# Performance work log

Measured on AMD Instinct MI355X. Metric: run time of the kernel, lower is better.

The kernel has to match this reference:

```python
import jax, jax.numpy as jnp
import numpy as np

N_NODES = 50000
NUM_FEATURES = 64
HIDDEN = 512
NUM_CLASSES = 2
N_EDGES = 800000
BN_EPS = 1e-5


def setup_inputs() -> dict:
    key = jax.random.key(0)
    ks = jax.random.split(key, 10)
    x = jax.random.normal(ks[0], (N_NODES, NUM_FEATURES), dtype=jnp.float32)
    edge_index = jax.random.randint(ks[1], (2, N_EDGES), 0, N_NODES, dtype=jnp.int64)
    # GINConv MLP: Linear(F,H) -> ReLU -> Linear(H,H)
    W1 = jax.random.normal(ks[2], (NUM_FEATURES, HIDDEN), dtype=jnp.float32) * 0.05
    b1 = jnp.zeros((HIDDEN,), dtype=jnp.float32)
    W2 = jax.random.normal(ks[3], (HIDDEN, HIDDEN), dtype=jnp.float32) * 0.05
    b2 = jnp.zeros((HIDDEN,), dtype=jnp.float32)
    # BatchNorm1d(HIDDEN) affine params
    gamma = jnp.ones((HIDDEN,), dtype=jnp.float32)
    beta = jnp.zeros((HIDDEN,), dtype=jnp.float32)
    # classifier: Linear(HIDDEN, NUM_CLASSES)
    Wc = jax.random.normal(ks[4], (HIDDEN, NUM_CLASSES), dtype=jnp.float32) * 0.05
    bc = jnp.zeros((NUM_CLASSES,), dtype=jnp.float32)
    return {"x": x, "edge_index": edge_index, "W1": W1, "b1": b1,
            "W2": W2, "b2": b2, "gamma": gamma, "beta": beta,
            "Wc": Wc, "bc": bc}


def reference(x, edge_index, W1, b1, W2, b2, gamma, beta, Wc, bc):
    # NOTE: the original torch forward returns inside the loop, so exactly ONE
    # GINConv layer runs, followed by batchnorm, relu, dropout(p=0), classifier.
    src, dst = edge_index[0], edge_index[1]
    # GINConv (eps=0): h_i = MLP(x_i + sum_{j -> i} x_j)
    agg = jax.ops.segment_sum(x[src], dst, num_segments=x.shape[0])  # [N, F]
    h = x + agg
    h = jax.nn.relu(h @ W1 + b1) @ W2 + b2  # [N, H]
    # BatchNorm1d in training mode: normalize with batch statistics (biased var)
    mean = jnp.mean(h, axis=0)
    var = jnp.var(h, axis=0)
    h = (h - mean) * jax.lax.rsqrt(var + BN_EPS) * gamma + beta
    h = jax.nn.relu(h)
    # dropout p=0.0 is a no-op
    return h @ Wc + bc  # [N, NUM_CLASSES]
```

## Files before the change

kernel.cpp:

```cpp
#include <hip/hip_runtime.h>
#include <hip/hip_bf16.h>

#define NN 50000
#define MP 50176
#define NF 64
#define NH 512
#define NE 800000
#define NBK 196
#define EBCAP 8192
#define ABLK 391
#define MB 392
#define GRID (MB * 4)
#define CPX (GRID / 8)

typedef __attribute__((ext_vector_type(8))) short bf16x8;
typedef __attribute__((ext_vector_type(4))) float f32x4;

#define GLOAD16(g, l)                                                        \
    __builtin_amdgcn_global_load_lds(                                        \
        (const __attribute__((address_space(1))) unsigned int*)(g),          \
        (__attribute__((address_space(3))) unsigned int*)(l), 16, 0, 0)

__global__ void detect_idx(const int* __restrict__ ei, int* __restrict__ flag) {
    if (threadIdx.x == 0 && blockIdx.x == 0) {
        int any = 0;
        for (int i = 0; i < 32; ++i) any |= ei[2 * i + 1];
        *flag = (any == 0) ? 1 : 0;
    }
}

__global__ __launch_bounds__(256) void bucketA(const void* __restrict__ eiv,
                                               const int* __restrict__ flag,
                                               int* __restrict__ bcnt,
                                               int* __restrict__ ebS,
                                               int* __restrict__ ebD) {
    __shared__ int hist[NBK];
    __shared__ int lcur[NBK];
    const int tid = threadIdx.x;
    const int chunk = blockIdx.x * 2048;
    const int lim = min(2048, NE - chunk);
    const bool is64 = (*flag != 0);
    const long long* ei64 = (const long long*)eiv;
    const int* ei32 = (const int*)eiv;

    for (int i = tid; i < NBK; i += 256) hist[i] = 0;
    __syncthreads();
    for (int i = tid; i < lim; i += 256) {
        int d = is64 ? (int)ei64[NE + chunk + i] : ei32[NE + chunk + i];
        atomicAdd(&hist[d >> 8], 1);
    }
    __syncthreads();
    for (int i = tid; i < NBK; i += 256) {
        int c = hist[i];
        lcur[i] = c ? atomicAdd(&bcnt[i], c) : 0;
    }
    __syncthreads();
    for (int i = tid; i < lim; i += 256) {
        int s, d;
        if (is64) { s = (int)ei64[chunk + i]; d = (int)ei64[NE + chunk + i]; }
        else      { s = ei32[chunk + i];      d = ei32[NE + chunk + i]; }
        int b = d >> 8;
        int p = atomicAdd(&lcur[b], 1);
        ebS[b * EBCAP + p] = s;
        ebD[b * EBCAP + p] = d;
    }
}

__global__ __launch_bounds__(256) void scan_bsum(const int* __restrict__ bsum,
                                                 int* __restrict__ boff) {
    __shared__ int sm[256];
    int tid = threadIdx.x;
    int v = (tid < NBK) ? bsum[tid] : 0;
    sm[tid] = v;
    __syncthreads();
    int acc = v;
#pragma unroll
    for (int off = 1; off < 256; off <<= 1) {
        int t = (tid >= off) ? sm[tid - off] : 0;
        __syncthreads();
        acc += t;
        sm[tid] = acc;
        __syncthreads();
    }
    if (tid < NBK) boff[tid] = acc - v;
}

__global__ __launch_bounds__(256) void bucketB(const int* __restrict__ ebS,
                                               const int* __restrict__ ebD,
                                               const int* __restrict__ bcnt,
                                               const int* __restrict__ bbase,
                                               int* __restrict__ rowptr,
                                               int* __restrict__ csr) {
    __shared__ int hist[256], sm[256], curs[256];
    const int b = blockIdx.x;
    const int tid = threadIdx.x;
    const int n0 = b << 8;
    const int cnt = bcnt[b];
    const int base = bbase[b];

    hist[tid] = 0;
    __syncthreads();
    for (int i = tid; i < cnt; i += 256)
        atomicAdd(&hist[ebD[b * EBCAP + i] & 255], 1);
    __syncthreads();
    int v = hist[tid];
    sm[tid] = v;
    __syncthreads();
    int acc = v;
#pragma unroll
    for (int off = 1; off < 256; off <<= 1) {
        int t = (tid >= off) ? sm[tid - off] : 0;
        __syncthreads();
        acc += t;
        sm[tid] = acc;
        __syncthreads();
    }
    int excl = acc - v;
    if (n0 + tid < NN) rowptr[n0 + tid] = base + excl;
    curs[tid] = excl;
    __syncthreads();
    for (int i = tid; i < cnt; i += 256) {
        int s = ebS[b * EBCAP + i];
        int d = ebD[b * EBCAP + i] & 255;
        int lp = atomicAdd(&curs[d], 1);
        csr[base + lp] = s;
    }
    if (b == 0 && tid == 0) rowptr[NN] = NE;
}

__global__ __launch_bounds__(256) void cvt_x(const float* __restrict__ x,
                                             __hip_bfloat16* __restrict__ xb) {
    int t = blockIdx.x * 256 + threadIdx.x;
    if (t >= NN * NF / 4) return;
    float4 v = *(const float4*)&x[t * 4];
    union { ushort4 u; __hip_bfloat16 h[4]; } o;
    o.h[0] = __float2bfloat16(v.x);
    o.h[1] = __float2bfloat16(v.y);
    o.h[2] = __float2bfloat16(v.z);
    o.h[3] = __float2bfloat16(v.w);
    *(ushort4*)&xb[t * 4] = o.u;
}

__global__ __launch_bounds__(256) void gather(const __hip_bfloat16* __restrict__ xb,
                                              const int* __restrict__ rowptr,
                                              const int* __restrict__ csr,
                                              __hip_bfloat16* __restrict__ h0b) {
    int n = blockIdx.x * 4 + (threadIdx.x >> 6);
    int lane = threadIdx.x & 63;
    if (n >= MP) return;
    if (n >= NN) {
        h0b[(long long)n * NF + lane] = __float2bfloat16(0.f);
        return;
    }
    float acc = __bfloat162float(xb[(long long)n * NF + lane]);
    int e = rowptr[n], e1 = rowptr[n + 1];
    for (; e + 4 <= e1; e += 4) {
        int s0 = csr[e], s1 = csr[e + 1], s2 = csr[e + 2], s3 = csr[e + 3];
        float v0 = __bfloat162float(xb[(long long)s0 * NF + lane]);
        float v1 = __bfloat162float(xb[(long long)s1 * NF + lane]);
        float v2 = __bfloat162float(xb[(long long)s2 * NF + lane]);
        float v3 = __bfloat162float(xb[(long long)s3 * NF + lane]);
        acc += (v0 + v1) + (v2 + v3);
    }
    for (; e < e1; ++e) acc += __bfloat162float(xb[(long long)csr[e] * NF + lane]);
    h0b[(long long)n * NF + lane] = __float2bfloat16(acc);
}

__global__ __launch_bounds__(256) void cvt_wt(const float* __restrict__ W,
                                              __hip_bfloat16* __restrict__ WT,
                                              int K, int N) {
    int t = blockIdx.x * 256 + threadIdx.x;
    if (t >= K * N) return;
    int n = t % N, k = t / N;
    WT[n * K + k] = __float2bfloat16(W[t]);
}

__global__ __launch_bounds__(256) void gemm1_direct(const __hip_bfloat16* __restrict__ A,
                                                    const __hip_bfloat16* __restrict__ BT,
                                                    const float* __restrict__ bias,
                                                    __hip_bfloat16* __restrict__ C) {
    const int orig = blockIdx.x;
    const int L = (orig & 7) * CPX + (orig >> 3);
    const int mb = L >> 2, nb = L & 3;

    const int tid = threadIdx.x;
    const int lane = tid & 63;
    const int w = tid >> 6;
    const int wm = w >> 1, wn = w & 1;
    const long long rbase = (long long)mb * 128;
    const int nbase = nb * 128;
    const int lo = lane & 15, hi = lane >> 4;

    f32x4 acc[4][4];
#pragma unroll
    for (int i = 0; i < 4; ++i)
#pragma unroll
        for (int j = 0; j < 4; ++j) acc[i][j] = (f32x4){0.f, 0.f, 0.f, 0.f};

#pragma unroll
    for (int ks = 0; ks < 2; ++ks) {
        bf16x8 af[4], bfr[4];
#pragma unroll
        for (int mi = 0; mi < 4; ++mi)
            af[mi] = *(const bf16x8*)&A[(rbase + wm * 64 + mi * 16 + lo) * NF +
                                        ks * 32 + hi * 8];
#pragma unroll
        for (int ni = 0; ni < 4; ++ni)
            bfr[ni] = *(const bf16x8*)&BT[(long long)(nbase + wn * 64 + ni * 16 + lo) * NF +
                                          ks * 32 + hi * 8];
#pragma unroll
        for (int mi = 0; mi < 4; ++mi)
#pragma unroll
            for (int ni = 0; ni < 4; ++ni)
                acc[mi][ni] = __builtin_amdgcn_mfma_f32_16x16x32_bf16(
                    af[mi], bfr[ni], acc[mi][ni], 0, 0, 0);
    }

    const int col0 = nbase + wn * 64 + lo;
    const long long row00 = rbase + wm * 64 + hi * 4;
#pragma unroll
    for (int ni = 0; ni < 4; ++ni) {
        int col = col0 + ni * 16;
        float bv = bias[col];
#pragma unroll
        for (int mi = 0; mi < 4; ++mi) {
            long long r0 = row00 + mi * 16;
#pragma unroll
            for (int r = 0; r < 4; ++r) {
                float v = fmaxf(acc[mi][ni][r] + bv, 0.f);
                C[(r0 + r) * NH + col] = __float2bfloat16(v);
            }
        }
    }
}

__global__ __launch_bounds__(256) void gemm2_db(const __hip_bfloat16* __restrict__ A,
                                                const __hip_bfloat16* __restrict__ BT,
                                                const float* __restrict__ bias,
                                                __hip_bfloat16* __restrict__ C,
                                                float* __restrict__ partial) {
    constexpr int BK = 64;
    __shared__ __align__(16) char smem[65536];
    float* smsum = (float*)smem;
    float* smsq  = (float*)(smem + 2048);

    const int orig = blockIdx.x;
    const int L = (orig & 7) * CPX + (orig >> 3);
    const int mb = L >> 2, nb = L & 3;

    const int tid = threadIdx.x;
    const int lane = tid & 63;
    const int w = tid >> 6;
    const int wm = w >> 1, wn = w & 1;
    const long long rbase = (long long)mb * 128;
    const int nbase = nb * 128;
    const int r8  = lane >> 3;
    const int swc = (lane & 7) ^ r8;
    const int key = lane & 7;
    const int lo = lane & 15, hi = lane >> 4;

    const __hip_bfloat16* gaBase =
        A + (rbase + w * 32 + r8) * (long long)NH + swc * 8;
    const __hip_bfloat16* gbBase =
        BT + (long long)(nbase + w * 32 + r8) * NH + swc * 8;
    const int laOff = (w * 32) * BK;

    auto STAGE = [&](int s, int kb) {
        __hip_bfloat16* la = (__hip_bfloat16*)(smem + s * 32768) + laOff;
        __hip_bfloat16* lb = (__hip_bfloat16*)(smem + s * 32768 + 16384) + laOff;
#pragma unroll
        for (int t = 0; t < 4; ++t)
            GLOAD16(gaBase + kb + (long long)t * 8 * NH, la + t * 8 * BK);
#pragma unroll
        for (int t = 0; t < 4; ++t)
            GLOAD16(gbBase + kb + (long long)t * 8 * NH, lb + t * 8 * BK);
    };

    f32x4 acc[4][4];
#pragma unroll
    for (int i = 0; i < 4; ++i)
#pragma unroll
        for (int j = 0; j < 4; ++j) acc[i][j] = (f32x4){0.f, 0.f, 0.f, 0.f};

    STAGE(0, 0);
    STAGE(1, BK);

#pragma unroll
    for (int t = 0; t < 8; ++t) {
        if (t == 7) { asm volatile("s_waitcnt vmcnt(0)" ::: "memory"); }
        else        { asm volatile("s_waitcnt vmcnt(8)" ::: "memory"); }
        __builtin_amdgcn_s_barrier();
        __builtin_amdgcn_sched_barrier(0);

        const __hip_bfloat16* Ac = (const __hip_bfloat16*)(smem + (t & 1) * 32768);
        const __hip_bfloat16* Bc = Ac + 8192;
#pragma unroll
        for (int ks = 0; ks < 2; ++ks) {
            bf16x8 af[4], bfr[4];
#pragma unroll
            for (int mi = 0; mi < 4; ++mi)
                af[mi] = *(const bf16x8*)&Ac[(wm * 64 + mi * 16 + lo) * BK +
                                             (((ks * 4 + hi) ^ key) * 8)];
#pragma unroll
            for (int ni = 0; ni < 4; ++ni)
                bfr[ni] = *(const bf16x8*)&Bc[(wn * 64 + ni * 16 + lo) * BK +
                                              (((ks * 4 + hi) ^ key) * 8)];
#pragma unroll
            for (int mi = 0; mi < 4; ++mi)
#pragma unroll
                for (int ni = 0; ni < 4; ++ni)
                    acc[mi][ni] = __builtin_amdgcn_mfma_f32_16x16x32_bf16(
                        af[mi], bfr[ni], acc[mi][ni], 0, 0, 0);
        }
        __builtin_amdgcn_sched_barrier(0);
        __builtin_amdgcn_s_barrier();
        __builtin_amdgcn_sched_barrier(0);
        if (t < 6) STAGE(t & 1, (t + 2) * BK);
    }

    __syncthreads();
    if (tid < 128) { smsum[tid] = 0.f; smsq[tid] = 0.f; }
    __syncthreads();
    const int col0 = nbase + wn * 64 + lo;
    const long long row00 = rbase + wm * 64 + hi * 4;
#pragma unroll
    for (int ni = 0; ni < 4; ++ni) {
        int col = col0 + ni * 16;
        float bv = bias[col];
        float s = 0.f, q = 0.f;
#pragma unroll
        for (int mi = 0; mi < 4; ++mi) {
            long long r0 = row00 + mi * 16;
#pragma unroll
            for (int r = 0; r < 4; ++r) {
                float v = acc[mi][ni][r] + bv;
                C[(r0 + r) * NH + col] = __float2bfloat16(v);
                if ((r0 + r) < NN) { s += v; q += v * v; }
            }
        }
        s += __shfl_xor(s, 16); s += __shfl_xor(s, 32);
        q += __shfl_xor(q, 16); q += __shfl_xor(q, 32);
        if (lane < 16) {
            atomicAdd(&smsum[wn * 64 + ni * 16 + lane], s);
            atomicAdd(&smsq[wn * 64 + ni * 16 + lane], q);
        }
    }
    __syncthreads();
    if (tid < 128) {
        partial[mb * 1024 + nbase + tid] = smsum[tid];
        partial[mb * 1024 + 512 + nbase + tid] = smsq[tid];
    }
}

__global__ __launch_bounds__(256) void stats_reduce(const float* __restrict__ partial,
                                                    float* __restrict__ stats) {
    int j = blockIdx.x * 256 + threadIdx.x;
    float s = 0.f;
    for (int mb = 0; mb < MB; ++mb) s += partial[mb * 1024 + j];
    stats[j] = s;
}

__global__ __launch_bounds__(256) void bn_cls(const __hip_bfloat16* __restrict__ h2b,
                                              const float* __restrict__ stats,
                                              const float* __restrict__ gamma,
                                              const float* __restrict__ beta,
                                              const float* __restrict__ Wc,
                                              const float* __restrict__ bc,
                                              float* __restrict__ out) {
    int tid = threadIdx.x;
    int lane = tid & 63;
    int k0 = lane * 8;
    float sc[8], sh[8], w0[8], w1[8];
#pragma unroll
    for (int j = 0; j < 8; ++j) {
        int k = k0 + j;
        float mean = stats[k] * (1.0f / NN);
        float var = stats[512 + k] * (1.0f / NN) - mean * mean;
        float rs = rsqrtf(var + 1e-5f);
        float s = gamma[k] * rs;
        sc[j] = s;
        sh[j] = beta[k] - mean * s;
        w0[j] = Wc[2 * k];
        w1[j] = Wc[2 * k + 1];
    }
    float bc0 = bc[0], bc1 = bc[1];
    int wid = blockIdx.x * 4 + (tid >> 6);
    int nw = gridDim.x * 4;
    for (int row = wid; row < NN; row += nw) {
        bf16x8 v8 = *(const bf16x8*)&h2b[(long long)row * NH + k0];
        float a0 = 0.f, a1 = 0.f;
#pragma unroll
        for (int j = 0; j < 8; ++j) {
            float v = __bfloat162float(((const __hip_bfloat16*)&v8)[j]);
            float hn = fmaxf(fmaf(v, sc[j], sh[j]), 0.f);
            a0 = fmaf(hn, w0[j], a0);
            a1 = fmaf(hn, w1[j], a1);
        }
#pragma unroll
        for (int off = 32; off; off >>= 1) {
            a0 += __shfl_xor(a0, off);
            a1 += __shfl_xor(a1, off);
        }
        if (lane == 0) {
            out[(long long)row * 2 + 0] = a0 + bc0;
            out[(long long)row * 2 + 1] = a1 + bc1;
        }
    }
}

extern "C" void kernel_launch(void* const* d_in, const int* in_sizes, int n_in,
                              void* d_out, int out_size, void* d_ws, size_t ws_size,
                              hipStream_t stream) {
    const float* x     = (const float*)d_in[0];
    const void*  ei    = d_in[1];
    const float* W1    = (const float*)d_in[2];
    const float* b1    = (const float*)d_in[3];
    const float* W2    = (const float*)d_in[4];
    const float* b2    = (const float*)d_in[5];
    const float* gamma = (const float*)d_in[6];
    const float* beta  = (const float*)d_in[7];
    const float* Wc    = (const float*)d_in[8];
    const float* bc    = (const float*)d_in[9];
    float* out = (float*)d_out;

    char* base = (char*)d_ws;
    size_t o = 0;
    auto alloc = [&](size_t bytes) {
        char* p = base + o;
        o = (o + bytes + 255) & ~(size_t)255;
        return p;
    };
    __hip_bfloat16* h0b     = (__hip_bfloat16*)alloc((size_t)MP * NF * 2);
    __hip_bfloat16* h1b     = (__hip_bfloat16*)alloc((size_t)MP * NH * 2);
    __hip_bfloat16* h2b     = (__hip_bfloat16*)alloc((size_t)MP * NH * 2);
    __hip_bfloat16* xb      = (__hip_bfloat16*)alloc((size_t)NN * NF * 2);
    __hip_bfloat16* w1t     = (__hip_bfloat16*)alloc((size_t)NH * NF * 2);
    __hip_bfloat16* w2t     = (__hip_bfloat16*)alloc((size_t)NH * NH * 2);
    int*            ebS     = (int*)alloc((size_t)NBK * EBCAP * 4);
    int*            ebD     = (int*)alloc((size_t)NBK * EBCAP * 4);
    int*            bcnt    = (int*)alloc(256 * 4);
    int*            bbase   = (int*)alloc(256 * 4);
    int*            rowptr  = (int*)alloc((size_t)(NN + 1) * 4);
    int*            csr     = (int*)alloc((size_t)NE * 4);
    float*          partial = (float*)alloc((size_t)MB * 1024 * 4);
    float*          stats   = (float*)alloc(1024 * 4);
    int*            flag    = (int*)alloc(256);

    hipMemsetAsync(bcnt, 0, NBK * 4, stream);
    detect_idx<<<1, 1, 0, stream>>>((const int*)ei, flag);

    bucketA<<<ABLK, 256, 0, stream>>>(ei, flag, bcnt, ebS, ebD);
    scan_bsum<<<1, 256, 0, stream>>>(bcnt, bbase);
    bucketB<<<NBK, 256, 0, stream>>>(ebS, ebD, bcnt, bbase, rowptr, csr);

    cvt_x<<<(NN * NF / 4 + 255) / 256, 256, 0, stream>>>(x, xb);
    gather<<<MP / 4, 256, 0, stream>>>(xb, rowptr, csr, h0b);

    cvt_wt<<<(NF * NH + 255) / 256, 256, 0, stream>>>(W1, w1t, NF, NH);
    cvt_wt<<<(NH * NH + 255) / 256, 256, 0, stream>>>(W2, w2t, NH, NH);

    gemm1_direct<<<GRID, 256, 0, stream>>>(h0b, w1t, b1, h1b);
    gemm2_db<<<GRID, 256, 0, stream>>>(h1b, w2t, b2, h2b, partial);

    stats_reduce<<<4, 256, 0, stream>>>(partial, stats);
    bn_cls<<<512, 256, 0, stream>>>(h2b, stats, gamma, beta, Wc, bc, out);
}
```

Before: 179.8 us.

## Pack edge bucket entries, merge conversion kernels, stage GEMM1 A tile in LDS

Bucketed edges are stored as one packed int (local dst in the high bits, src in the low 16 bits) instead of two separate arrays, which halves bucket traffic. The x, W1 and W2 bf16 conversions are merged into one launch to save launch overhead. GEMM1 now loads its A tile into swizzled LDS with async global-to-LDS copies and preloads the B fragments into registers. Packing src into 16 bits is only correct for node indices below 65536, so it relies on N_NODES=50000.

```diff
diff --git a/kernel.cpp b/kernel.cpp
--- a/kernel.cpp
+++ b/kernel.cpp
@@ -32,8 +32,7 @@
 __global__ __launch_bounds__(256) void bucketA(const void* __restrict__ eiv,
                                                const int* __restrict__ flag,
                                                int* __restrict__ bcnt,
-                                               int* __restrict__ ebS,
-                                               int* __restrict__ ebD) {
+                                               int* __restrict__ ebP) {
     __shared__ int hist[NBK];
     __shared__ int lcur[NBK];
     const int tid = threadIdx.x;
@@ -61,8 +60,7 @@
         else      { s = ei32[chunk + i];      d = ei32[NE + chunk + i]; }
         int b = d >> 8;
         int p = atomicAdd(&lcur[b], 1);
-        ebS[b * EBCAP + p] = s;
-        ebD[b * EBCAP + p] = d;
+        ebP[b * EBCAP + p] = ((d & 255) << 16) | s;
     }
 }
 
@@ -85,8 +83,7 @@
     if (tid < NBK) boff[tid] = acc - v;
 }
 
-__global__ __launch_bounds__(256) void bucketB(const int* __restrict__ ebS,
-                                               const int* __restrict__ ebD,
+__global__ __launch_bounds__(256) void bucketB(const int* __restrict__ ebP,
                                                const int* __restrict__ bcnt,
                                                const int* __restrict__ bbase,
                                                int* __restrict__ rowptr,
@@ -101,7 +98,7 @@
     hist[tid] = 0;
     __syncthreads();
     for (int i = tid; i < cnt; i += 256)
-        atomicAdd(&hist[ebD[b * EBCAP + i] & 255], 1);
+        atomicAdd(&hist[(ebP[b * EBCAP + i] >> 16) & 255], 1);
     __syncthreads();
     int v = hist[tid];
     sm[tid] = v;
@@ -120,25 +117,41 @@
     curs[tid] = excl;
     __syncthreads();
     for (int i = tid; i < cnt; i += 256) {
-        int s = ebS[b * EBCAP + i];
-        int d = ebD[b * EBCAP + i] & 255;
-        int lp = atomicAdd(&curs[d], 1);
-        csr[base + lp] = s;
+        int p = ebP[b * EBCAP + i];
+        int lp = atomicAdd(&curs[(p >> 16) & 255], 1);
+        csr[base + lp] = p & 0xFFFF;
     }
     if (b == 0 && tid == 0) rowptr[NN] = NE;
 }
 
-__global__ __launch_bounds__(256) void cvt_x(const float* __restrict__ x,
-                                             __hip_bfloat16* __restrict__ xb) {
-    int t = blockIdx.x * 256 + threadIdx.x;
-    if (t >= NN * NF / 4) return;
-    float4 v = *(const float4*)&x[t * 4];
-    union { ushort4 u; __hip_bfloat16 h[4]; } o;
-    o.h[0] = __float2bfloat16(v.x);
-    o.h[1] = __float2bfloat16(v.y);
-    o.h[2] = __float2bfloat16(v.z);
-    o.h[3] = __float2bfloat16(v.w);
-    *(ushort4*)&xb[t * 4] = o.u;
+#define XBLK  (NN * NF / 4 / 256)
+#define W1BLK (NF * NH / 256)
+#define W2BLK (NH * NH / 256)
+__global__ __launch_bounds__(256) void cvt_all(const float* __restrict__ x,
+                                               const float* __restrict__ W1,
+                                               const float* __restrict__ W2,
+                                               __hip_bfloat16* __restrict__ xb,
+                                               __hip_bfloat16* __restrict__ w1t,
+                                               __hip_bfloat16* __restrict__ w2t) {
+    int bb = blockIdx.x;
+    if (bb < XBLK) {
+        int t = bb * 256 + threadIdx.x;
+        float4 v = *(const float4*)&x[t * 4];
+        union { ushort4 u; __hip_bfloat16 h[4]; } o;
+        o.h[0] = __float2bfloat16(v.x);
+        o.h[1] = __float2bfloat16(v.y);
+        o.h[2] = __float2bfloat16(v.z);
+        o.h[3] = __float2bfloat16(v.w);
+        *(ushort4*)&xb[t * 4] = o.u;
+    } else if (bb < XBLK + W1BLK) {
+        int t = (bb - XBLK) * 256 + threadIdx.x;
+        int n = t % NH, k = t / NH;
+        w1t[n * NF + k] = __float2bfloat16(W1[t]);
+    } else {
+        int t = (bb - XBLK - W1BLK) * 256 + threadIdx.x;
+        int n = t % NH, k = t / NH;
+        w2t[n * NH + k] = __float2bfloat16(W2[t]);
+    }
 }
 
 __global__ __launch_bounds__(256) void gather(const __hip_bfloat16* __restrict__ xb,
@@ -166,19 +179,11 @@
     h0b[(long long)n * NF + lane] = __float2bfloat16(acc);
 }
 
-__global__ __launch_bounds__(256) void cvt_wt(const float* __restrict__ W,
-                                              __hip_bfloat16* __restrict__ WT,
-                                              int K, int N) {
-    int t = blockIdx.x * 256 + threadIdx.x;
-    if (t >= K * N) return;
-    int n = t % N, k = t / N;
-    WT[n * K + k] = __float2bfloat16(W[t]);
-}
-
-__global__ __launch_bounds__(256) void gemm1_direct(const __hip_bfloat16* __restrict__ A,
+__global__ __launch_bounds__(256) void gemm1_staged(const __hip_bfloat16* __restrict__ A,
                                                     const __hip_bfloat16* __restrict__ BT,
                                                     const float* __restrict__ bias,
                                                     __hip_bfloat16* __restrict__ C) {
+    __shared__ __hip_bfloat16 As[128 * 64];
     const int orig = blockIdx.x;
     const int L = (orig & 7) * CPX + (orig >> 3);
     const int mb = L >> 2, nb = L & 3;
@@ -189,8 +194,27 @@
     const int wm = w >> 1, wn = w & 1;
     const long long rbase = (long long)mb * 128;
     const int nbase = nb * 128;
+    const int r8  = lane >> 3;
+    const int swc = (lane & 7) ^ r8;
+    const int key = lane & 7;
     const int lo = lane & 15, hi = lane >> 4;
 
+    {
+        const __hip_bfloat16* ga = A + (rbase + w * 32 + r8) * NF + swc * 8;
+        __hip_bfloat16* la = As + (w * 32) * 64;
+#pragma unroll
+        for (int t = 0; t < 4; ++t)
+            GLOAD16(ga + t * 8 * NF, la + t * 8 * 64);
+    }
+    bf16x8 bfr[2][4];
+#pragma unroll
+    for (int ks = 0; ks < 2; ++ks)
+#pragma unroll
+        for (int ni = 0; ni < 4; ++ni)
+            bfr[ks][ni] = *(const bf16x8*)&BT[(nbase + wn * 64 + ni * 16 + lo) * NF +
+                                             ks * 32 + hi * 8];
+    __syncthreads();
+
     f32x4 acc[4][4];
 #pragma unroll
     for (int i = 0; i < 4; ++i)
@@ -199,21 +223,17 @@
 
 #pragma unroll
     for (int ks = 0; ks < 2; ++ks) {
-        bf16x8 af[4], bfr[4];
+        bf16x8 af[4];
 #pragma unroll
         for (int mi = 0; mi < 4; ++mi)
-            af[mi] = *(const bf16x8*)&A[(rbase + wm * 64 + mi * 16 + lo) * NF +
-                                        ks * 32 + hi * 8];
-#pragma unroll
-        for (int ni = 0; ni < 4; ++ni)
-            bfr[ni] = *(const bf16x8*)&BT[(long long)(nbase + wn * 64 + ni * 16 + lo) * NF +
-                                          ks * 32 + hi * 8];
+            af[mi] = *(const bf16x8*)&As[(wm * 64 + mi * 16 + lo) * 64 +
+                                         (((ks * 4 + hi) ^ key) * 8)];
 #pragma unroll
         for (int mi = 0; mi < 4; ++mi)
 #pragma unroll
             for (int ni = 0; ni < 4; ++ni)
                 acc[mi][ni] = __builtin_amdgcn_mfma_f32_16x16x32_bf16(
-                    af[mi], bfr[ni], acc[mi][ni], 0, 0, 0);
+                    af[mi], bfr[ks][ni], acc[mi][ni], 0, 0, 0);
     }
 
     const int col0 = nbase + wn * 64 + lo;
@@ -436,8 +456,7 @@
     __hip_bfloat16* xb      = (__hip_bfloat16*)alloc((size_t)NN * NF * 2);
     __hip_bfloat16* w1t     = (__hip_bfloat16*)alloc((size_t)NH * NF * 2);
     __hip_bfloat16* w2t     = (__hip_bfloat16*)alloc((size_t)NH * NH * 2);
-    int*            ebS     = (int*)alloc((size_t)NBK * EBCAP * 4);
-    int*            ebD     = (int*)alloc((size_t)NBK * EBCAP * 4);
+    int*            ebP     = (int*)alloc((size_t)NBK * EBCAP * 4);
     int*            bcnt    = (int*)alloc(256 * 4);
     int*            bbase   = (int*)alloc(256 * 4);
     int*            rowptr  = (int*)alloc((size_t)(NN + 1) * 4);
@@ -449,17 +468,14 @@
     hipMemsetAsync(bcnt, 0, NBK * 4, stream);
     detect_idx<<<1, 1, 0, stream>>>((const int*)ei, flag);
 
-    bucketA<<<ABLK, 256, 0, stream>>>(ei, flag, bcnt, ebS, ebD);
+    bucketA<<<ABLK, 256, 0, stream>>>(ei, flag, bcnt, ebP);
     scan_bsum<<<1, 256, 0, stream>>>(bcnt, bbase);
-    bucketB<<<NBK, 256, 0, stream>>>(ebS, ebD, bcnt, bbase, rowptr, csr);
-
-    cvt_x<<<(NN * NF / 4 + 255) / 256, 256, 0, stream>>>(x, xb);
+    bucketB<<<NBK, 256, 0, stream>>>(ebP, bcnt, bbase, rowptr, csr);
+
+    cvt_all<<<XBLK + W1BLK + W2BLK, 256, 0, stream>>>(x, W1, W2, xb, w1t, w2t);
     gather<<<MP / 4, 256, 0, stream>>>(xb, rowptr, csr, h0b);
 
-    cvt_wt<<<(NF * NH + 255) / 256, 256, 0, stream>>>(W1, w1t, NF, NH);
-    cvt_wt<<<(NH * NH + 255) / 256, 256, 0, stream>>>(W2, w2t, NH, NH);
-
-    gemm1_direct<<<GRID, 256, 0, stream>>>(h0b, w1t, b1, h1b);
+    gemm1_staged<<<GRID, 256, 0, stream>>>(h0b, w1t, b1, h1b);
     gemm2_db<<<GRID, 256, 0, stream>>>(h1b, w2t, b2, h2b, partial);
 
     stats_reduce<<<4, 256, 0, stream>>>(partial, stats);
```

Result: faster. 167.4 us (-6.9%).
